# Performance work log

Hardware: AMD Instinct MI355X
Metric: run time of the kernel (lower is better)

The kernel has to match this reference:

```python
import jax, jax.numpy as jnp
import numpy as np

T, B, N, DIN, H, DOUT = 20, 32, 100, 2, 128, 2
BN = B * N


def setup_inputs() -> dict:
    key = jax.random.key(0)
    ks = jax.random.split(key, 12)
    x = jax.random.normal(ks[0], (T, BN, DIN), jnp.float32)
    A = jax.random.randint(ks[1], (T, BN, BN), 0, 2, jnp.int32)
    mask = jax.random.randint(ks[2], (T, BN), 0, 2, jnp.int32).astype(bool)
    s_g = 1.0 / np.sqrt(DIN)
    s_h = 1.0 / np.sqrt(H)
    u = lambda k, shp, s: jax.random.uniform(k, shp, jnp.float32, -s, s)
    return {
        'x': x, 'A': A, 'mask': mask, 'num_nodes': N,
        'W_gcn': u(ks[3], (DIN, H), s_g), 'b_gcn': jnp.zeros((H,), jnp.float32),
        'W_ih': u(ks[4], (H, 3 * H), s_h), 'b_ih': u(ks[5], (3 * H,), s_h),
        'W_hh': u(ks[6], (H, 3 * H), s_h), 'b_hh': u(ks[7], (3 * H,), s_h),
        'W_fc': u(ks[8], (H, DOUT), s_h), 'b_fc': u(ks[9], (DOUT,), s_h),
    }


def reference(x, A, mask, num_nodes, W_gcn, b_gcn, W_ih, b_ih, W_hh, b_hh, W_fc, b_fc):
    BN_ = x.shape[1]
    B_ = BN_ // num_nodes

    def step(h, inp):
        feats, A_t, m_t = inp
        mf = m_t.astype(jnp.float32)
        # masked subgraph adjacency + self loops only on masked nodes (PyG add_self_loops on subgraph)
        Ahat = A_t.astype(jnp.float32) * mf[:, None] * mf[None, :] + jnp.diag(mf)
        deg = Ahat.sum(axis=0)  # PyG gcn_norm: in-degree at edge_index[1] (column sum)
        dinv = jnp.where(deg > 0, jax.lax.rsqrt(deg), 0.0)
        xw = feats @ W_gcn  # [BN, H]
        # out[i] = dinv[i] * sum_j Ahat[j,i] * dinv[j] * xw[j]
        agg = dinv[:, None] * (Ahat.T @ (xw * dinv[:, None]))
        g = jax.nn.relu(agg + b_gcn)
        # torch GRUCell
        gi = g @ W_ih + b_ih
        gh = h @ W_hh + b_hh
        ir, iz, ig = jnp.split(gi, 3, axis=-1)
        hr, hz, hg = jnp.split(gh, 3, axis=-1)
        r = jax.nn.sigmoid(ir + hr)
        z = jax.nn.sigmoid(iz + hz)
        n = jnp.tanh(ig + r * hg)
        h_new = (1.0 - z) * n + z * h
        h = jnp.where(m_t[:, None], h_new, h)  # scatter-back: only masked nodes update
        return h, h

    h0 = jnp.zeros((BN_, H), jnp.float32)
    _, seq = jax.lax.scan(step, h0, (x, A, mask))  # [T, BN, H]
    seq = seq.reshape(x.shape[0], B_, num_nodes, H)
    out = seq @ W_fc + b_fc  # [T, B, N, DOUT]
    return out.transpose(1, 2, 0, 3)  # [B, N, T, DOUT]
```

## Files before the change

kernel.cpp:

```cpp
#include <hip/hip_runtime.h>
#include <math.h>

#define T_  20
#define BN  3200
#define H   128
#define N3H 384
#define DOUT 2
#define JW  400

typedef unsigned char u8;

__device__ __forceinline__ bool getm(const u8* m8, const int* m32, int fl, int idx) {
    return fl ? (m8[idx] != 0) : (m32[idx] != 0);
}

__global__ void k_detect(const u8* __restrict__ mask, int* __restrict__ flag) {
    int i = blockIdx.x * 256 + threadIdx.x;
    bool hit = (i < T_ * BN) && (i & 3) && (mask[i] != 0);
    if (__any(hit) && (threadIdx.x & 63) == 0) atomicOr(flag, 1);
}

__global__ void k_compact(const u8* __restrict__ m8, const int* __restrict__ m32,
                          const int* __restrict__ flag,
                          int* __restrict__ act_idx, int* __restrict__ act_cnt) {
    int t = blockIdx.x, fl = *flag;
    for (int j = threadIdx.x; j < BN; j += blockDim.x) {
        if (getm(m8, m32, fl, t * BN + j)) {
            int pos = atomicAdd(&act_cnt[t], 1);
            act_idx[t * BN + pos] = j;
        }
    }
}

__global__ __launch_bounds__(256) void k_deg_pack(const int* __restrict__ A,
                                                  const int* __restrict__ act_idx,
                                                  const int* __restrict__ act_cnt,
                                                  u8* __restrict__ A1,
                                                  int* __restrict__ deg) {
    int t = blockIdx.z, rc = blockIdx.y;
    int c = blockIdx.x * 256 + threadIdx.x;
    if (c >= BN) return;
    int nact = act_cnt[t];
    int start = rc * 128;
    if (start >= nact) return;
    int end = min(start + 128, nact);
    const int* At = A + (size_t)t * BN * BN;
    const int* ai = act_idx + t * BN;
    int cnt = 0;
    for (int jb = start; jb < end; jb += 8) {
        unsigned byte = 0;
        int lim = min(8, end - jb);
        #pragma unroll
        for (int q = 0; q < 8; ++q) {
            if (q < lim) {
                int j = ai[jb + q];
                int a = At[(size_t)j * BN + c];
                cnt += a;
                byte |= (unsigned)a << q;
            }
        }
        A1[((size_t)t * JW + (jb >> 3)) * BN + c] = (u8)byte;
    }
    atomicAdd(&deg[t * BN + c], cnt);
}

__global__ void k_dinv(const int* __restrict__ deg, const u8* __restrict__ m8,
                       const int* __restrict__ m32, const int* __restrict__ flag,
                       float* __restrict__ dinv) {
    int i = blockIdx.x * 256 + threadIdx.x;
    int fl = *flag;
    dinv[i] = getm(m8, m32, fl, i) ? rsqrtf((float)(deg[i] + 1)) : 0.f;
}

__global__ void k_u(const float* __restrict__ x, const float* __restrict__ dinv,
                    const int* __restrict__ act_idx, const int* __restrict__ act_cnt,
                    float* __restrict__ u0c, float* __restrict__ u1c) {
    int idx = blockIdx.x * 256 + threadIdx.x;
    int t = idx / BN, jj = idx - t * BN;
    float v0 = 0.f, v1 = 0.f;
    if (jj < act_cnt[t]) {
        int j = act_idx[t * BN + jj];
        float d = dinv[t * BN + j];
        v0 = d * x[(size_t)(t * BN + j) * 2];
        v1 = d * x[(size_t)(t * BN + j) * 2 + 1];
    }
    u0c[idx] = v0;
    u1c[idx] = v1;
}

__global__ __launch_bounds__(256) void k_c(const u8* __restrict__ A1,
                                           const int* __restrict__ act_cnt,
                                           const float* __restrict__ u0c,
                                           const float* __restrict__ u1c,
                                           float* __restrict__ c0g,
                                           float* __restrict__ c1g) {
    int t = blockIdx.z, js = blockIdx.y;
    int c = blockIdx.x * 1024 + threadIdx.x * 4;
    if (c >= BN) return;
    int nactp = (act_cnt[t] + 7) >> 3;
    int jw0 = js * (JW / 8), jw1 = min(jw0 + JW / 8, nactp);
    if (jw0 >= jw1) return;
    const u8* base = A1 + (size_t)t * JW * BN;
    const float* U0 = u0c + t * BN;
    const float* U1 = u1c + t * BN;
    float s0[4] = {0.f, 0.f, 0.f, 0.f}, s1[4] = {0.f, 0.f, 0.f, 0.f};
    for (int jw = jw0; jw < jw1; ++jw) {
        uchar4 aa = *(const uchar4*)(base + (size_t)jw * BN + c);
        unsigned bb[4] = {aa.x, aa.y, aa.z, aa.w};
        const float* Up0 = U0 + jw * 8;
        const float* Up1 = U1 + jw * 8;
        #pragma unroll
        for (int jb = 0; jb < 8; ++jb) {
            float w0 = Up0[jb], w1 = Up1[jb];
            #pragma unroll
            for (int k = 0; k < 4; ++k) {
                if ((bb[k] >> jb) & 1) { s0[k] += w0; s1[k] += w1; }
            }
        }
    }
    #pragma unroll
    for (int k = 0; k < 4; ++k) {
        atomicAdd(&c0g[t * BN + c + k], s0[k]);
        atomicAdd(&c1g[t * BN + c + k], s1[k]);
    }
}

__global__ __launch_bounds__(128) void k_gi(const float* __restrict__ dinv,
                                            const float* __restrict__ c0g,
                                            const float* __restrict__ c1g,
                                            const float* __restrict__ x,
                                            const float* __restrict__ Wg,
                                            const float* __restrict__ bg,
                                            const u8* __restrict__ m8,
                                            const int* __restrict__ m32,
                                            const int* __restrict__ flag,
                                            const float* __restrict__ Wih,
                                            const float* __restrict__ bih,
                                            float* __restrict__ GI) {
    int row0 = blockIdx.x * 16;
    int tid = threadIdx.x;
    __shared__ float gs[16][H];
    __shared__ float e0s[16], e1s[16];
    __shared__ int msh[16];
    if (tid < 16) {
        int row = row0 + tid;
        msh[tid] = getm(m8, m32, *flag, row) ? 1 : 0;
        float d = dinv[row];
        e0s[tid] = d * (c0g[row] + d * x[(size_t)row * 2]);
        e1s[tid] = d * (c1g[row] + d * x[(size_t)row * 2 + 1]);
    }
    __syncthreads();
    float wg0 = Wg[tid], wg1 = Wg[H + tid], bgv = bg[tid];
    #pragma unroll
    for (int r = 0; r < 16; ++r)
        gs[r][tid] = fmaxf(e0s[r] * wg0 + e1s[r] * wg1 + bgv, 0.f);
    __syncthreads();

    float acc[16][3];
    #pragma unroll
    for (int r = 0; r < 16; ++r) { acc[r][0] = 0.f; acc[r][1] = 0.f; acc[r][2] = 0.f; }

    for (int k = 0; k < H; k += 4) {
        float w[4][3];
        #pragma unroll
        for (int kk = 0; kk < 4; ++kk) {
            const float* wr = Wih + (size_t)(k + kk) * N3H;
            w[kk][0] = wr[tid]; w[kk][1] = wr[128 + tid]; w[kk][2] = wr[256 + tid];
        }
        #pragma unroll
        for (int r = 0; r < 16; ++r) {
            if (!msh[r]) continue;
            float4 g4 = *(const float4*)&gs[r][k];
            acc[r][0] += g4.x * w[0][0] + g4.y * w[1][0] + g4.z * w[2][0] + g4.w * w[3][0];
            acc[r][1] += g4.x * w[0][1] + g4.y * w[1][1] + g4.z * w[2][1] + g4.w * w[3][1];
            acc[r][2] += g4.x * w[0][2] + g4.y * w[1][2] + g4.z * w[2][2] + g4.w * w[3][2];
        }
    }
    float b0 = bih[tid], b1 = bih[128 + tid], b2 = bih[256 + tid];
    #pragma unroll
    for (int r = 0; r < 16; ++r) {
        if (!msh[r]) continue;
        size_t bbase = (size_t)(row0 + r) * N3H;
        GI[bbase + tid]       = acc[r][0] + b0;
        GI[bbase + 128 + tid] = acc[r][1] + b1;
        GI[bbase + 256 + tid] = acc[r][2] + b2;
    }
}

__global__ __launch_bounds__(256) void k_gru(const float* __restrict__ GI,
                                             const float* __restrict__ Whh,
                                             const float* __restrict__ bhh,
                                             const u8* __restrict__ m8,
                                             const int* __restrict__ m32,
                                             const int* __restrict__ flag,
                                             const float* __restrict__ Wfc,
                                             const float* __restrict__ bfc,
                                             float* __restrict__ out) {
    int row0 = blockIdx.x * 16;
    int tid = threadIdx.x;
    int u = tid & 127, half = tid >> 7;
    int fl = *flag;
    __shared__ float hs[16][H];
    __shared__ int ms[16];
    __shared__ float red[4][8][2];
    for (int idx = tid; idx < 16 * H; idx += 256) (&hs[0][0])[idx] = 0.f;

    float b0 = bhh[u], b1 = bhh[128 + u], b2 = bhh[256 + u];
    float wf0 = Wfc[u * 2], wf1 = Wfc[u * 2 + 1];
    float bf0 = bfc[0], bf1 = bfc[1];
    int wv = tid >> 6;

    for (int t = 0; t < T_; ++t) {
        if (tid < 16) ms[tid] = getm(m8, m32, fl, t * BN + row0 + tid) ? 1 : 0;
        __syncthreads();

        float a0[8], a1[8], a2[8];
        #pragma unroll
        for (int r = 0; r < 8; ++r) { a0[r] = 0.f; a1[r] = 0.f; a2[r] = 0.f; }

        for (int k = 0; k < H; k += 4) {
            float w[4][3];
            #pragma unroll
            for (int kk = 0; kk < 4; ++kk) {
                const float* wr = Whh + (size_t)(k + kk) * N3H;
                w[kk][0] = wr[u]; w[kk][1] = wr[128 + u]; w[kk][2] = wr[256 + u];
            }
            #pragma unroll
            for (int r = 0; r < 8; ++r) {
                int gr = half * 8 + r;
                if (!ms[gr]) continue;
                float4 h4 = *(const float4*)&hs[gr][k];
                a0[r] += h4.x * w[0][0] + h4.y * w[1][0] + h4.z * w[2][0] + h4.w * w[3][0];
                a1[r] += h4.x * w[0][1] + h4.y * w[1][1] + h4.z * w[2][1] + h4.w * w[3][1];
                a2[r] += h4.x * w[0][2] + h4.y * w[1][2] + h4.z * w[2][2] + h4.w * w[3][2];
            }
        }
        #pragma unroll
        for (int r = 0; r < 8; ++r) {
            int gr = half * 8 + r;
            if (!ms[gr]) continue;
            size_t gb = ((size_t)t * BN + row0 + gr) * N3H;
            float ir = GI[gb + u], iz = GI[gb + 128 + u], ig = GI[gb + 256 + u];
            float rg = 1.f / (1.f + expf(-(ir + a0[r] + b0)));
            float zg = 1.f / (1.f + expf(-(iz + a1[r] + b1)));
            float ng = tanhf(ig + rg * (a2[r] + b2));
            hs[gr][u] = (1.f - zg) * ng + zg * hs[gr][u];
        }
        #pragma unroll
        for (int r = 0; r < 8; ++r) {
            int gr = half * 8 + r;
            float hv = hs[gr][u];
            float p0 = hv * wf0, p1 = hv * wf1;
            for (int o = 32; o > 0; o >>= 1) { p0 += __shfl_down(p0, o); p1 += __shfl_down(p1, o); }
            if ((tid & 63) == 0) { red[wv][r][0] = p0; red[wv][r][1] = p1; }
        }
        __syncthreads();
        if (tid < 32) {
            int gr = tid >> 1, d = tid & 1;
            int wbase = (gr >> 3) * 2, rr = gr & 7;
            float val = red[wbase][rr][d] + red[wbase + 1][rr][d] + (d ? bf1 : bf0);
            out[((size_t)(row0 + gr) * T_ + t) * DOUT + d] = val;
        }
        __syncthreads();
    }
}

extern "C" void kernel_launch(void* const* d_in, const int* in_sizes, int n_in,
                              void* d_out, int out_size, void* d_ws, size_t ws_size,
                              hipStream_t stream) {
    const float* x    = (const float*)d_in[0];
    const int*   A    = (const int*)d_in[1];
    const u8*    m8   = (const u8*)d_in[2];
    const int*   m32  = (const int*)d_in[2];
    const float* Wg   = (const float*)d_in[4];
    const float* bg   = (const float*)d_in[5];
    const float* Wih  = (const float*)d_in[6];
    const float* bih  = (const float*)d_in[7];
    const float* Whh  = (const float*)d_in[8];
    const float* bhh  = (const float*)d_in[9];
    const float* Wfc  = (const float*)d_in[10];
    const float* bfc  = (const float*)d_in[11];
    float* out = (float*)d_out;

    char* ws = (char*)d_ws;
    size_t off = 0;
    auto alloc = [&](size_t bytes) {
        void* p = ws + off;
        off += (bytes + 255) & ~(size_t)255;
        return p;
    };
    int*   flag    = (int*)alloc(4);
    int*   act_cnt = (int*)alloc(T_ * 4);
    int*   deg     = (int*)alloc((size_t)T_ * BN * 4);
    float* c0g     = (float*)alloc((size_t)T_ * BN * 4);
    float* c1g     = (float*)alloc((size_t)T_ * BN * 4);
    size_t zbytes = off;
    int*   act_idx = (int*)alloc((size_t)T_ * BN * 4);
    float* dinv    = (float*)alloc((size_t)T_ * BN * 4);
    float* u0c     = (float*)alloc((size_t)T_ * BN * 4);
    float* u1c     = (float*)alloc((size_t)T_ * BN * 4);
    u8*    A1      = (u8*)alloc((size_t)T_ * JW * BN);
    float* GI      = (float*)alloc((size_t)T_ * BN * N3H * 4);

    hipMemsetAsync(ws, 0, zbytes, stream);
    k_detect<<<(T_ * BN + 255) / 256, 256, 0, stream>>>(m8, flag);
    k_compact<<<T_, 256, 0, stream>>>(m8, m32, flag, act_idx, act_cnt);
    k_deg_pack<<<dim3((BN + 255) / 256, BN / 128, T_), 256, 0, stream>>>(A, act_idx, act_cnt, A1, deg);
    k_dinv<<<(T_ * BN) / 256, 256, 0, stream>>>(deg, m8, m32, flag, dinv);
    k_u<<<(T_ * BN) / 256, 256, 0, stream>>>(x, dinv, act_idx, act_cnt, u0c, u1c);
    k_c<<<dim3(4, 8, T_), 256, 0, stream>>>(A1, act_cnt, u0c, u1c, c0g, c1g);
    k_gi<<<(T_ * BN) / 16, 128, 0, stream>>>(dinv, c0g, c1g, x, Wg, bg, m8, m32, flag, Wih, bih, GI);
    k_gru<<<BN / 16, 256, 0, stream>>>(GI, Whh, bhh, m8, m32, flag, Wfc, bfc, out);
}
```

Measured before the change: 1.645 ms.

## Vectorize adjacency packing, compact GI rows, fuse small kernels, restructure GRU

The degree/pack kernel now reads four adjacency columns per thread with int4 loads and stages active indices in shared memory. The input-gate GEMM runs only over compacted active rows, with 384 threads so each thread owns one output column. Mask-type detection is folded into the compaction kernel, and dinv is fused with the u computation. The GRU kernel computes the hidden-gate products into shared memory with 384 threads and splits the gate math and the output projection into separate phases. These changes target uncoalesced or scalar traffic on the large adjacency tensor and wasted work on inactive rows, at the cost of more shared memory and extra barriers per timestep.

```diff
diff --git a/kernel.cpp b/kernel.cpp
--- a/kernel.cpp
+++ b/kernel.cpp
@@ -14,17 +14,24 @@
     return fl ? (m8[idx] != 0) : (m32[idx] != 0);
 }
 
-__global__ void k_detect(const u8* __restrict__ mask, int* __restrict__ flag) {
-    int i = blockIdx.x * 256 + threadIdx.x;
-    bool hit = (i < T_ * BN) && (i & 3) && (mask[i] != 0);
-    if (__any(hit) && (threadIdx.x & 63) == 0) atomicOr(flag, 1);
-}
-
-__global__ void k_compact(const u8* __restrict__ m8, const int* __restrict__ m32,
-                          const int* __restrict__ flag,
-                          int* __restrict__ act_idx, int* __restrict__ act_cnt) {
-    int t = blockIdx.x, fl = *flag;
-    for (int j = threadIdx.x; j < BN; j += blockDim.x) {
+__global__ __launch_bounds__(256) void k_compact(const u8* __restrict__ m8,
+                                                 const int* __restrict__ m32,
+                                                 int* __restrict__ flag,
+                                                 int* __restrict__ act_idx,
+                                                 int* __restrict__ act_cnt) {
+    int t = blockIdx.x, tid = threadIdx.x;
+    __shared__ int lf;
+    if (tid == 0) lf = 0;
+    __syncthreads();
+    bool hit = false;
+    for (int j = tid; j < BN; j += 256) {
+        if ((j & 3) && m8[t * BN + j]) hit = true;
+    }
+    if (__any(hit) && (tid & 63) == 0) atomicOr(&lf, 1);
+    __syncthreads();
+    int fl = lf;
+    if (tid == 0 && fl) atomicOr(flag, 1);
+    for (int j = tid; j < BN; j += 256) {
         if (getm(m8, m32, fl, t * BN + j)) {
             int pos = atomicAdd(&act_cnt[t], 1);
             act_idx[t * BN + pos] = j;
@@ -32,55 +39,80 @@
     }
 }
 
+#define RCH 256
 __global__ __launch_bounds__(256) void k_deg_pack(const int* __restrict__ A,
                                                   const int* __restrict__ act_idx,
                                                   const int* __restrict__ act_cnt,
                                                   u8* __restrict__ A1,
                                                   int* __restrict__ deg) {
-    int t = blockIdx.z, rc = blockIdx.y;
-    int c = blockIdx.x * 256 + threadIdx.x;
+    int t = blockIdx.z;
+    int nact = act_cnt[t];
+    int start = blockIdx.y * RCH;
+    if (start >= nact) return;
+    int n = min(RCH, nact - start);
+    __shared__ int ai_s[RCH];
+    int tid = threadIdx.x;
+    if (tid < n) ai_s[tid] = act_idx[t * BN + start + tid];
+    __syncthreads();
+
+    int c = (blockIdx.x * 256 + tid) * 4;
     if (c >= BN) return;
-    int nact = act_cnt[t];
-    int start = rc * 128;
-    if (start >= nact) return;
-    int end = min(start + 128, nact);
     const int* At = A + (size_t)t * BN * BN;
-    const int* ai = act_idx + t * BN;
-    int cnt = 0;
-    for (int jb = start; jb < end; jb += 8) {
-        unsigned byte = 0;
-        int lim = min(8, end - jb);
+    u8* A1t = A1 + ((size_t)t * JW + (start >> 3)) * BN + c;
+    int cnt0 = 0, cnt1 = 0, cnt2 = 0, cnt3 = 0;
+    int n8 = n & ~7;
+    int jb = 0;
+    for (; jb < n8; jb += 8) {
+        unsigned b0 = 0, b1 = 0, b2 = 0, b3 = 0;
         #pragma unroll
         for (int q = 0; q < 8; ++q) {
-            if (q < lim) {
-                int j = ai[jb + q];
-                int a = At[(size_t)j * BN + c];
-                cnt += a;
-                byte |= (unsigned)a << q;
-            }
-        }
-        A1[((size_t)t * JW + (jb >> 3)) * BN + c] = (u8)byte;
-    }
-    atomicAdd(&deg[t * BN + c], cnt);
-}
-
-__global__ void k_dinv(const int* __restrict__ deg, const u8* __restrict__ m8,
-                       const int* __restrict__ m32, const int* __restrict__ flag,
-                       float* __restrict__ dinv) {
-    int i = blockIdx.x * 256 + threadIdx.x;
+            int j = ai_s[jb + q];
+            int4 aa = *(const int4*)(At + (size_t)j * BN + c);
+            cnt0 += aa.x; b0 |= (unsigned)aa.x << q;
+            cnt1 += aa.y; b1 |= (unsigned)aa.y << q;
+            cnt2 += aa.z; b2 |= (unsigned)aa.z << q;
+            cnt3 += aa.w; b3 |= (unsigned)aa.w << q;
+        }
+        uchar4 pk; pk.x = (u8)b0; pk.y = (u8)b1; pk.z = (u8)b2; pk.w = (u8)b3;
+        *(uchar4*)(A1t + (size_t)(jb >> 3) * BN) = pk;
+    }
+    if (jb < n) {
+        unsigned b0 = 0, b1 = 0, b2 = 0, b3 = 0;
+        for (int q = 0; q < n - jb; ++q) {
+            int j = ai_s[jb + q];
+            int4 aa = *(const int4*)(At + (size_t)j * BN + c);
+            cnt0 += aa.x; b0 |= (unsigned)aa.x << q;
+            cnt1 += aa.y; b1 |= (unsigned)aa.y << q;
+            cnt2 += aa.z; b2 |= (unsigned)aa.z << q;
+            cnt3 += aa.w; b3 |= (unsigned)aa.w << q;
+        }
+        uchar4 pk; pk.x = (u8)b0; pk.y = (u8)b1; pk.z = (u8)b2; pk.w = (u8)b3;
+        *(uchar4*)(A1t + (size_t)(jb >> 3) * BN) = pk;
+    }
+    atomicAdd(&deg[t * BN + c], cnt0);
+    atomicAdd(&deg[t * BN + c + 1], cnt1);
+    atomicAdd(&deg[t * BN + c + 2], cnt2);
+    atomicAdd(&deg[t * BN + c + 3], cnt3);
+}
+
+__global__ __launch_bounds__(256) void k_dinv_u(const int* __restrict__ deg,
+                                                const u8* __restrict__ m8,
+                                                const int* __restrict__ m32,
+                                                const int* __restrict__ flag,
+                                                const float* __restrict__ x,
+                                                const int* __restrict__ act_idx,
+                                                const int* __restrict__ act_cnt,
+                                                float* __restrict__ dinv,
+                                                float* __restrict__ u0c,
+                                                float* __restrict__ u1c) {
+    int idx = blockIdx.x * 256 + threadIdx.x;
     int fl = *flag;
-    dinv[i] = getm(m8, m32, fl, i) ? rsqrtf((float)(deg[i] + 1)) : 0.f;
-}
-
-__global__ void k_u(const float* __restrict__ x, const float* __restrict__ dinv,
-                    const int* __restrict__ act_idx, const int* __restrict__ act_cnt,
-                    float* __restrict__ u0c, float* __restrict__ u1c) {
-    int idx = blockIdx.x * 256 + threadIdx.x;
-    int t = idx / BN, jj = idx - t * BN;
+    int t = idx / BN, r = idx - t * BN;
+    dinv[idx] = getm(m8, m32, fl, idx) ? rsqrtf((float)(deg[idx] + 1)) : 0.f;
     float v0 = 0.f, v1 = 0.f;
-    if (jj < act_cnt[t]) {
-        int j = act_idx[t * BN + jj];
-        float d = dinv[t * BN + j];
+    if (r < act_cnt[t]) {
+        int j = act_idx[idx];
+        float d = rsqrtf((float)(deg[t * BN + j] + 1));
         v0 = d * x[(size_t)(t * BN + j) * 2];
         v1 = d * x[(size_t)(t * BN + j) * 2 + 1];
     }
@@ -88,6 +120,7 @@
     u1c[idx] = v1;
 }
 
+#define JSL 25
 __global__ __launch_bounds__(256) void k_c(const u8* __restrict__ A1,
                                            const int* __restrict__ act_cnt,
                                            const float* __restrict__ u0c,
@@ -98,7 +131,7 @@
     int c = blockIdx.x * 1024 + threadIdx.x * 4;
     if (c >= BN) return;
     int nactp = (act_cnt[t] + 7) >> 3;
-    int jw0 = js * (JW / 8), jw1 = min(jw0 + JW / 8, nactp);
+    int jw0 = js * JSL, jw1 = min(jw0 + JSL, nactp);
     if (jw0 >= jw1) return;
     const u8* base = A1 + (size_t)t * JW * BN;
     const float* U0 = u0c + t * BN;
@@ -125,69 +158,67 @@
     }
 }
 
-__global__ __launch_bounds__(128) void k_gi(const float* __restrict__ dinv,
+__global__ __launch_bounds__(384) void k_gi(const float* __restrict__ dinv,
                                             const float* __restrict__ c0g,
                                             const float* __restrict__ c1g,
                                             const float* __restrict__ x,
                                             const float* __restrict__ Wg,
                                             const float* __restrict__ bg,
-                                            const u8* __restrict__ m8,
-                                            const int* __restrict__ m32,
-                                            const int* __restrict__ flag,
+                                            const int* __restrict__ act_idx,
+                                            const int* __restrict__ act_cnt,
                                             const float* __restrict__ Wih,
                                             const float* __restrict__ bih,
                                             float* __restrict__ GI) {
-    int row0 = blockIdx.x * 16;
+    int t = blockIdx.y;
+    int nact = act_cnt[t];
+    int sb = blockIdx.x * 32;
+    if (sb >= nact) return;
+    int ns = min(32, nact - sb);
+    __shared__ float gs[32][H];
+    __shared__ float e0s[32], e1s[32];
+    __shared__ int ar[32];
     int tid = threadIdx.x;
-    __shared__ float gs[16][H];
-    __shared__ float e0s[16], e1s[16];
-    __shared__ int msh[16];
-    if (tid < 16) {
-        int row = row0 + tid;
-        msh[tid] = getm(m8, m32, *flag, row) ? 1 : 0;
-        float d = dinv[row];
-        e0s[tid] = d * (c0g[row] + d * x[(size_t)row * 2]);
-        e1s[tid] = d * (c1g[row] + d * x[(size_t)row * 2 + 1]);
-    }
-    __syncthreads();
-    float wg0 = Wg[tid], wg1 = Wg[H + tid], bgv = bg[tid];
+    if (tid < 32) {
+        int row = 0; float e0 = 0.f, e1 = 0.f;
+        if (tid < ns) {
+            row = act_idx[t * BN + sb + tid];
+            int gi = t * BN + row;
+            float d = dinv[gi];
+            e0 = d * (c0g[gi] + d * x[(size_t)gi * 2]);
+            e1 = d * (c1g[gi] + d * x[(size_t)gi * 2 + 1]);
+        }
+        ar[tid] = row; e0s[tid] = e0; e1s[tid] = e1;
+    }
+    __syncthreads();
+    for (int u2 = tid; u2 < 32 * H; u2 += 384) {
+        int r = u2 >> 7, h = u2 & 127;
+        gs[r][h] = fmaxf(e0s[r] * Wg[h] + e1s[r] * Wg[H + h] + bg[h], 0.f);
+    }
+    __syncthreads();
+
+    float acc[32];
     #pragma unroll
-    for (int r = 0; r < 16; ++r)
-        gs[r][tid] = fmaxf(e0s[r] * wg0 + e1s[r] * wg1 + bgv, 0.f);
-    __syncthreads();
-
-    float acc[16][3];
+    for (int r = 0; r < 32; ++r) acc[r] = 0.f;
+    for (int k = 0; k < H; k += 4) {
+        float w0 = Wih[(size_t)k * N3H + tid];
+        float w1 = Wih[(size_t)(k + 1) * N3H + tid];
+        float w2 = Wih[(size_t)(k + 2) * N3H + tid];
+        float w3 = Wih[(size_t)(k + 3) * N3H + tid];
+        #pragma unroll
+        for (int r = 0; r < 32; ++r) {
+            float4 g4 = *(const float4*)&gs[r][k];
+            acc[r] += g4.x * w0 + g4.y * w1 + g4.z * w2 + g4.w * w3;
+        }
+    }
+    float bb = bih[tid];
     #pragma unroll
-    for (int r = 0; r < 16; ++r) { acc[r][0] = 0.f; acc[r][1] = 0.f; acc[r][2] = 0.f; }
-
-    for (int k = 0; k < H; k += 4) {
-        float w[4][3];
-        #pragma unroll
-        for (int kk = 0; kk < 4; ++kk) {
-            const float* wr = Wih + (size_t)(k + kk) * N3H;
-            w[kk][0] = wr[tid]; w[kk][1] = wr[128 + tid]; w[kk][2] = wr[256 + tid];
-        }
-        #pragma unroll
-        for (int r = 0; r < 16; ++r) {
-            if (!msh[r]) continue;
-            float4 g4 = *(const float4*)&gs[r][k];
-            acc[r][0] += g4.x * w[0][0] + g4.y * w[1][0] + g4.z * w[2][0] + g4.w * w[3][0];
-            acc[r][1] += g4.x * w[0][1] + g4.y * w[1][1] + g4.z * w[2][1] + g4.w * w[3][1];
-            acc[r][2] += g4.x * w[0][2] + g4.y * w[1][2] + g4.z * w[2][2] + g4.w * w[3][2];
-        }
-    }
-    float b0 = bih[tid], b1 = bih[128 + tid], b2 = bih[256 + tid];
-    #pragma unroll
-    for (int r = 0; r < 16; ++r) {
-        if (!msh[r]) continue;
-        size_t bbase = (size_t)(row0 + r) * N3H;
-        GI[bbase + tid]       = acc[r][0] + b0;
-        GI[bbase + 128 + tid] = acc[r][1] + b1;
-        GI[bbase + 256 + tid] = acc[r][2] + b2;
-    }
-}
-
-__global__ __launch_bounds__(256) void k_gru(const float* __restrict__ GI,
+    for (int r = 0; r < 32; ++r) {
+        if (r < ns)
+            GI[((size_t)t * BN + ar[r]) * N3H + tid] = acc[r] + bb;
+    }
+}
+
+__global__ __launch_bounds__(384) void k_gru(const float* __restrict__ GI,
                                              const float* __restrict__ Whh,
                                              const float* __restrict__ bhh,
                                              const u8* __restrict__ m8,
@@ -198,68 +229,88 @@
                                              float* __restrict__ out) {
     int row0 = blockIdx.x * 16;
     int tid = threadIdx.x;
-    int u = tid & 127, half = tid >> 7;
     int fl = *flag;
     __shared__ float hs[16][H];
+    __shared__ float ghs[16][N3H];
+    __shared__ float bhs[N3H];
     __shared__ int ms[16];
-    __shared__ float red[4][8][2];
-    for (int idx = tid; idx < 16 * H; idx += 256) (&hs[0][0])[idx] = 0.f;
-
-    float b0 = bhh[u], b1 = bhh[128 + u], b2 = bhh[256 + u];
-    float wf0 = Wfc[u * 2], wf1 = Wfc[u * 2 + 1];
+    for (int i = tid; i < 16 * H; i += 384) (&hs[0][0])[i] = 0.f;
+    if (tid < N3H) bhs[tid] = bhh[tid];
+    int lane = tid & 63, wv = tid >> 6;
+    float wfa0 = Wfc[lane * 2],        wfa1 = Wfc[lane * 2 + 1];
+    float wfb0 = Wfc[(lane + 64) * 2], wfb1 = Wfc[(lane + 64) * 2 + 1];
     float bf0 = bfc[0], bf1 = bfc[1];
-    int wv = tid >> 6;
 
     for (int t = 0; t < T_; ++t) {
         if (tid < 16) ms[tid] = getm(m8, m32, fl, t * BN + row0 + tid) ? 1 : 0;
         __syncthreads();
-
-        float a0[8], a1[8], a2[8];
-        #pragma unroll
-        for (int r = 0; r < 8; ++r) { a0[r] = 0.f; a1[r] = 0.f; a2[r] = 0.f; }
-
+        int mrl[16];
+        #pragma unroll
+        for (int r = 0; r < 16; ++r) mrl[r] = ms[r];
+
+        float pir[6], piz[6], pig[6];
+        #pragma unroll
+        for (int ii = 0; ii < 6; ++ii) {
+            pir[ii] = 0.f; piz[ii] = 0.f; pig[ii] = 0.f;
+            int i5 = tid + ii * 384;
+            if (i5 < 16 * H) {
+                int r = i5 >> 7, u = i5 & 127;
+                if (ms[r]) {
+                    size_t gb = ((size_t)t * BN + row0 + r) * N3H;
+                    pir[ii] = GI[gb + u];
+                    piz[ii] = GI[gb + 128 + u];
+                    pig[ii] = GI[gb + 256 + u];
+                }
+            }
+        }
+
+        float acc[16];
+        #pragma unroll
+        for (int r = 0; r < 16; ++r) acc[r] = 0.f;
         for (int k = 0; k < H; k += 4) {
-            float w[4][3];
+            float w0 = Whh[(size_t)k * N3H + tid];
+            float w1 = Whh[(size_t)(k + 1) * N3H + tid];
+            float w2 = Whh[(size_t)(k + 2) * N3H + tid];
+            float w3 = Whh[(size_t)(k + 3) * N3H + tid];
             #pragma unroll
-            for (int kk = 0; kk < 4; ++kk) {
-                const float* wr = Whh + (size_t)(k + kk) * N3H;
-                w[kk][0] = wr[u]; w[kk][1] = wr[128 + u]; w[kk][2] = wr[256 + u];
-            }
-            #pragma unroll
-            for (int r = 0; r < 8; ++r) {
-                int gr = half * 8 + r;
-                if (!ms[gr]) continue;
-                float4 h4 = *(const float4*)&hs[gr][k];
-                a0[r] += h4.x * w[0][0] + h4.y * w[1][0] + h4.z * w[2][0] + h4.w * w[3][0];
-                a1[r] += h4.x * w[0][1] + h4.y * w[1][1] + h4.z * w[2][1] + h4.w * w[3][1];
-                a2[r] += h4.x * w[0][2] + h4.y * w[1][2] + h4.z * w[2][2] + h4.w * w[3][2];
-            }
-        }
-        #pragma unroll
-        for (int r = 0; r < 8; ++r) {
-            int gr = half * 8 + r;
-            if (!ms[gr]) continue;
-            size_t gb = ((size_t)t * BN + row0 + gr) * N3H;
-            float ir = GI[gb + u], iz = GI[gb + 128 + u], ig = GI[gb + 256 + u];
-            float rg = 1.f / (1.f + expf(-(ir + a0[r] + b0)));
-            float zg = 1.f / (1.f + expf(-(iz + a1[r] + b1)));
-            float ng = tanhf(ig + rg * (a2[r] + b2));
-            hs[gr][u] = (1.f - zg) * ng + zg * hs[gr][u];
-        }
-        #pragma unroll
-        for (int r = 0; r < 8; ++r) {
-            int gr = half * 8 + r;
-            float hv = hs[gr][u];
-            float p0 = hv * wf0, p1 = hv * wf1;
+            for (int r = 0; r < 16; ++r) {
+                if (mrl[r]) {
+                    float4 h4 = *(const float4*)&hs[r][k];
+                    acc[r] += h4.x * w0 + h4.y * w1 + h4.z * w2 + h4.w * w3;
+                }
+            }
+        }
+        #pragma unroll
+        for (int r = 0; r < 16; ++r) ghs[r][tid] = acc[r];
+        __syncthreads();
+
+        #pragma unroll
+        for (int ii = 0; ii < 6; ++ii) {
+            int i5 = tid + ii * 384;
+            if (i5 < 16 * H) {
+                int r = i5 >> 7, u = i5 & 127;
+                if (ms[r]) {
+                    float hr = ghs[r][u] + bhs[u];
+                    float hz = ghs[r][128 + u] + bhs[128 + u];
+                    float hg = ghs[r][256 + u] + bhs[256 + u];
+                    float rg = 1.f / (1.f + expf(-(pir[ii] + hr)));
+                    float zg = 1.f / (1.f + expf(-(piz[ii] + hz)));
+                    float ng = tanhf(pig[ii] + rg * hg);
+                    hs[r][u] = (1.f - zg) * ng + zg * hs[r][u];
+                }
+            }
+        }
+        __syncthreads();
+
+        for (int r = wv; r < 16; r += 6) {
+            float h0 = hs[r][lane], h1 = hs[r][lane + 64];
+            float p0 = h0 * wfa0 + h1 * wfb0;
+            float p1 = h0 * wfa1 + h1 * wfb1;
             for (int o = 32; o > 0; o >>= 1) { p0 += __shfl_down(p0, o); p1 += __shfl_down(p1, o); }
-            if ((tid & 63) == 0) { red[wv][r][0] = p0; red[wv][r][1] = p1; }
-        }
-        __syncthreads();
-        if (tid < 32) {
-            int gr = tid >> 1, d = tid & 1;
-            int wbase = (gr >> 3) * 2, rr = gr & 7;
-            float val = red[wbase][rr][d] + red[wbase + 1][rr][d] + (d ? bf1 : bf0);
-            out[((size_t)(row0 + gr) * T_ + t) * DOUT + d] = val;
+            if (lane == 0) {
+                out[((size_t)(row0 + r) * T_ + t) * DOUT]     = p0 + bf0;
+                out[((size_t)(row0 + r) * T_ + t) * DOUT + 1] = p1 + bf1;
+            }
         }
         __syncthreads();
     }
@@ -303,12 +354,10 @@
     float* GI      = (float*)alloc((size_t)T_ * BN * N3H * 4);
 
     hipMemsetAsync(ws, 0, zbytes, stream);
-    k_detect<<<(T_ * BN + 255) / 256, 256, 0, stream>>>(m8, flag);
     k_compact<<<T_, 256, 0, stream>>>(m8, m32, flag, act_idx, act_cnt);
-    k_deg_pack<<<dim3((BN + 255) / 256, BN / 128, T_), 256, 0, stream>>>(A, act_idx, act_cnt, A1, deg);
-    k_dinv<<<(T_ * BN) / 256, 256, 0, stream>>>(deg, m8, m32, flag, dinv);
-    k_u<<<(T_ * BN) / 256, 256, 0, stream>>>(x, dinv, act_idx, act_cnt, u0c, u1c);
-    k_c<<<dim3(4, 8, T_), 256, 0, stream>>>(A1, act_cnt, u0c, u1c, c0g, c1g);
-    k_gi<<<(T_ * BN) / 16, 128, 0, stream>>>(dinv, c0g, c1g, x, Wg, bg, m8, m32, flag, Wih, bih, GI);
-    k_gru<<<BN / 16, 256, 0, stream>>>(GI, Whh, bhh, m8, m32, flag, Wfc, bfc, out);
-}
+    k_deg_pack<<<dim3(4, 13, T_), 256, 0, stream>>>(A, act_idx, act_cnt, A1, deg);
+    k_dinv_u<<<(T_ * BN) / 256, 256, 0, stream>>>(deg, m8, m32, flag, x, act_idx, act_cnt, dinv, u0c, u1c);
+    k_c<<<dim3(4, 16, T_), 256, 0, stream>>>(A1, act_cnt, u0c, u1c, c0g, c1g);
+    k_gi<<<dim3(100, T_), 384, 0, stream>>>(dinv, c0g, c1g, x, Wg, bg, act_idx, act_cnt, Wih, bih, GI);
+    k_gru<<<BN / 16, 384, 0, stream>>>(GI, Whh, bhh, m8, m32, flag, Wfc, bfc, out);
+}
```

After: 1.639 ms. No clear change (-0.4%).
